# Kernel optimization log

Hardware: AMD Instinct MI355X
Metric: run time of the kernel (lower is better)

The kernel has to match this reference:

```python
import jax, jax.numpy as jnp
import numpy as np

VOCAB = 32000; DIM = 512; NL = 6; B = 2; L = 1024
DI = 2 * DIM      # d_inner (expand=2)
DS = 16           # d_state
DC = 4            # d_conv
DR = DIM // 16    # dt_rank = ceil(512/16) = 32


def setup_inputs() -> dict:
    key = jax.random.key(0)
    ks = jax.random.split(key, 10)
    s = 0.02
    tokens = jax.random.randint(ks[0], (B, L), 0, VOCAB)
    pos_emb = jax.random.normal(ks[1], (1, L, DIM)) * s
    embed = jax.random.normal(ks[2], (VOCAB, DIM)) * s
    lm_w = jax.random.normal(ks[3], (VOCAB, DIM)) * s
    lm_b = jnp.zeros((VOCAB,), jnp.float32)
    in_proj_w = jax.random.normal(ks[4], (NL, 2 * DI, DIM)) * s
    conv_w = jax.random.normal(ks[5], (NL, DI, DC)) * s
    conv_b = jnp.zeros((NL, DI), jnp.float32)
    x_proj_w = jax.random.normal(ks[6], (NL, DR + 2 * DS, DI)) * s
    dt_proj_w = jax.random.normal(ks[7], (NL, DI, DR)) * s
    dt_proj_b = jnp.broadcast_to(jnp.log(jnp.expm1(jnp.float32(0.01))), (NL, DI)).astype(jnp.float32)
    A_log = jnp.log(jnp.broadcast_to(jnp.arange(1, DS + 1, dtype=jnp.float32), (NL, DI, DS)))
    Dp = jnp.ones((NL, DI), jnp.float32)
    out_w = jax.random.normal(ks[8], (NL, DIM, DI)) * s
    ln_g = jnp.ones((NL, DIM), jnp.float32)
    ln_b = jnp.zeros((NL, DIM), jnp.float32)
    return dict(tokens=tokens, pos_emb=pos_emb, embed=embed, lm_w=lm_w, lm_b=lm_b,
                in_proj_w=in_proj_w, conv_w=conv_w, conv_b=conv_b, x_proj_w=x_proj_w,
                dt_proj_w=dt_proj_w, dt_proj_b=dt_proj_b, A_log=A_log, Dp=Dp,
                out_w=out_w, ln_g=ln_g, ln_b=ln_b)


def silu(x):
    return x * jax.nn.sigmoid(x)


def layernorm(x, g, b, eps=1e-5):
    mu = jnp.mean(x, -1, keepdims=True)
    var = jnp.var(x, -1, keepdims=True)
    return (x - mu) * jax.lax.rsqrt(var + eps) * g + b


def causal_dwconv(x, w, b):
    # x: (B,L,DI), w: (DI,DC) depthwise, left-pad causal
    xp = jnp.pad(x, ((0, 0), (DC - 1, 0), (0, 0)))
    y = b
    for k in range(DC):
        y = y + w[:, k] * xp[:, k:k + x.shape[1], :]
    return y


def selective_scan(u, dt, A, Bm, Cm, Dp):
    # u,dt: (B,L,DI); A: (DI,DS); Bm,Cm: (B,L,DS)
    dA = jnp.exp(dt[..., None] * A)                       # (B,L,DI,DS)
    dBu = dt[..., None] * Bm[:, :, None, :] * u[..., None]
    h0 = jnp.zeros((u.shape[0], DI, DS), u.dtype)

    def step(h, inp):
        dA_t, dBu_t, C_t = inp
        h = dA_t * h + dBu_t
        y = jnp.einsum('bdn,bn->bd', h, C_t)
        return h, y

    _, ys = jax.lax.scan(step, h0, (dA.transpose(1, 0, 2, 3),
                                    dBu.transpose(1, 0, 2, 3),
                                    Cm.transpose(1, 0, 2)))
    return ys.transpose(1, 0, 2) + u * Dp


def mamba_block(x, in_w, cw, cb, xp_w, dtw, dtb, A_log, Dp, ow):
    xz = jnp.einsum('bld,ed->ble', x, in_w)               # (B,L,2*DI)
    xc, z = jnp.split(xz, 2, axis=-1)
    xc = silu(causal_dwconv(xc, cw, cb))
    x_dbl = jnp.einsum('bld,ed->ble', xc, xp_w)           # (B,L,DR+2*DS)
    dt, Bm, Cm = jnp.split(x_dbl, [DR, DR + DS], axis=-1)
    dt = jax.nn.softplus(jnp.einsum('blr,dr->bld', dt, dtw) + dtb)
    A = -jnp.exp(A_log)
    y = selective_scan(xc, dt, A, Bm, Cm, Dp)
    y = y * silu(z)
    return jnp.einsum('bld,ed->ble', y, ow)


def reference(tokens, pos_emb, embed, lm_w, lm_b, in_proj_w, conv_w, conv_b,
              x_proj_w, dt_proj_w, dt_proj_b, A_log, Dp, out_w, ln_g, ln_b):
    x = embed[tokens] + pos_emb[:, :tokens.shape[1]]
    for i in range(NL):
        res = x
        x = mamba_block(x, in_proj_w[i], conv_w[i], conv_b[i], x_proj_w[i],
                        dt_proj_w[i], dt_proj_b[i], A_log[i], Dp[i], out_w[i])
        x = layernorm(x + res, ln_g[i], ln_b[i])
    return jnp.einsum('bld,vd->blv', x, lm_w) + lm_b
```

## Files before the change

### kernel.cpp

```cpp
#include <hip/hip_runtime.h>
#include <hip/hip_bf16.h>
#include <math.h>

#define BB 2
#define LL 1024
#define DIM 512
#define NL 6
#define DI 1024
#define DS 16
#define DC 4
#define DR 32
#define VOCAB 32000
#define M_ROWS (BB * LL)
#define CCH 64
#define CHLEN (LL / CCH)
#define KSPLIT 8
#define OSPLIT 4

typedef unsigned short u16;
typedef __attribute__((ext_vector_type(8))) short bf16x8;
typedef __attribute__((ext_vector_type(4))) float f32x4;

__device__ __forceinline__ u16 f2bf(float f) {
    unsigned u = __float_as_uint(f);
    u += 0x7FFF + ((u >> 16) & 1);
    return (u16)(u >> 16);
}
__device__ __forceinline__ float bf2f(u16 h) {
    return __uint_as_float(((unsigned)h) << 16);
}
#define SWZ(r, c) ((c) ^ (((r) >> 1) & 3))

__global__ __launch_bounds__(256) void cast_all(const float* __restrict__ lm,
                                                const float* __restrict__ inw,
                                                const float* __restrict__ ow,
                                                const float* __restrict__ xp,
                                                u16* __restrict__ lmb,
                                                u16* __restrict__ inb,
                                                u16* __restrict__ owb_,
                                                u16* __restrict__ xpb) {
    int idx = blockIdx.x * 256 + threadIdx.x;
    const float* src; u16* dst; int off;
    if (idx < 2048000)      { src = lm;  dst = lmb;  off = idx; }
    else if (idx < 2834432) { src = inw; dst = inb;  off = idx - 2048000; }
    else if (idx < 3227648) { src = ow;  dst = owb_; off = idx - 2834432; }
    else                    { src = xp;  dst = xpb;  off = idx - 3227648; }
    float4 v0 = ((const float4*)src)[off * 2];
    float4 v1 = ((const float4*)src)[off * 2 + 1];
    union { u16 h[8]; int4 v; } r;
    r.h[0] = f2bf(v0.x); r.h[1] = f2bf(v0.y); r.h[2] = f2bf(v0.z); r.h[3] = f2bf(v0.w);
    r.h[4] = f2bf(v1.x); r.h[5] = f2bf(v1.y); r.h[6] = f2bf(v1.z); r.h[7] = f2bf(v1.w);
    ((int4*)dst)[off] = r.v;
}

__global__ __launch_bounds__(256) void embed_kernel(const int* __restrict__ tok,
                                                    const float* __restrict__ pos,
                                                    const float* __restrict__ emb,
                                                    float* __restrict__ x,
                                                    u16* __restrict__ xb) {
    int idx = blockIdx.x * 256 + threadIdx.x;
    int d = idx & (DIM - 1);
    int l = (idx >> 9) & (LL - 1);
    int b = idx >> 19;
    int t = tok[b * LL + l];
    float v = emb[(size_t)t * DIM + d] + pos[l * DIM + d];
    x[idx] = v;
    xb[idx] = f2bf(v);
}

__global__ __launch_bounds__(256) void gemm_n64(const u16* __restrict__ A,
                                                const u16* __restrict__ W,
                                                float* __restrict__ out,
                                                u16* __restrict__ outb,
                                                const float* __restrict__ bias,
                                                int lda, int ldw, int ldc,
                                                int KS, int pstride) {
    __shared__ __align__(16) u16 As[2 * 4096];
    __shared__ __align__(16) u16 Ws[2 * 2048];
    const int t = threadIdx.x;
    const int l = t & 63;
    const int w = t >> 6;
    const int kz = blockIdx.x;
    const int bm = blockIdx.y * 128;
    const int bnn = blockIdx.z * 64;
    const int wm = w * 32;

    f32x4 acc[2][4] = {};
    const int nt = KS >> 5;
    const int kbeg = kz * KS;

    auto STAGE = [&](int bufi, int k0) {
#pragma unroll
        for (int p = 0; p < 2; ++p) {
            const int i = p * 256 + w * 64 + l;
            const int row = i >> 2;
            const int kq = SWZ(row, i & 3);
            __builtin_amdgcn_global_load_lds(
                (const __attribute__((address_space(1))) unsigned int*)
                    (A + (size_t)(bm + row) * lda + k0 + kq * 8),
                (__attribute__((address_space(3))) unsigned int*)
                    (As + bufi * 4096 + (p * 256 + w * 64) * 8),
                16, 0, 0);
        }
        {
            const int i = w * 64 + l;
            const int row = i >> 2;
            const int kq = SWZ(row, i & 3);
            __builtin_amdgcn_global_load_lds(
                (const __attribute__((address_space(1))) unsigned int*)
                    (W + (size_t)(bnn + row) * ldw + k0 + kq * 8),
                (__attribute__((address_space(3))) unsigned int*)
                    (Ws + bufi * 2048 + (w * 64) * 8),
                16, 0, 0);
        }
    };
    auto COMPUTE = [&](int bufi) {
        const u16* Ab = As + bufi * 4096;
        const u16* Wb = Ws + bufi * 2048;
#pragma unroll
        for (int mi = 0; mi < 2; ++mi) {
            const int ar = wm + mi * 16 + (l & 15);
            bf16x8 a = *(const bf16x8*)(Ab + ar * 32 + SWZ(ar, l >> 4) * 8);
#pragma unroll
            for (int ni = 0; ni < 4; ++ni) {
                const int wr = ni * 16 + (l & 15);
                bf16x8 b = *(const bf16x8*)(Wb + wr * 32 + SWZ(wr, l >> 4) * 8);
                acc[mi][ni] = __builtin_amdgcn_mfma_f32_16x16x32_bf16(b, a, acc[mi][ni], 0, 0, 0);
            }
        }
    };

    STAGE(0, kbeg);
    for (int tt = 0; tt < nt; ++tt) {
        if (tt + 1 < nt) {
            STAGE((tt + 1) & 1, kbeg + ((tt + 1) << 5));
            asm volatile("s_waitcnt vmcnt(3)\ns_barrier" ::: "memory");
        } else {
            asm volatile("s_waitcnt vmcnt(0)\ns_barrier" ::: "memory");
        }
        COMPUTE(tt & 1);
        asm volatile("s_waitcnt lgkmcnt(0)\ns_barrier" ::: "memory");
    }

    if (outb != nullptr) {
        u16* opb = outb + (size_t)kz * pstride;
#pragma unroll
        for (int mi = 0; mi < 2; ++mi) {
            const int row = bm + wm + mi * 16 + (l & 15);
#pragma unroll
            for (int ni = 0; ni < 4; ++ni) {
                const int col = bnn + ni * 16 + ((l >> 4) << 2);
                ushort4 v;
                v.x = f2bf(acc[mi][ni][0]); v.y = f2bf(acc[mi][ni][1]);
                v.z = f2bf(acc[mi][ni][2]); v.w = f2bf(acc[mi][ni][3]);
                *(ushort4*)(opb + (size_t)row * ldc + col) = v;
            }
        }
    } else {
        float* op = out + (size_t)kz * pstride;
#pragma unroll
        for (int mi = 0; mi < 2; ++mi) {
            const int row = bm + wm + mi * 16 + (l & 15);
#pragma unroll
            for (int ni = 0; ni < 4; ++ni) {
                const int col = bnn + ni * 16 + ((l >> 4) << 2);
                float4 v;
                v.x = acc[mi][ni][0]; v.y = acc[mi][ni][1];
                v.z = acc[mi][ni][2]; v.w = acc[mi][ni][3];
                if (bias != nullptr) {
                    float4 b4 = *(const float4*)(bias + col);
                    v.x += b4.x; v.y += b4.y; v.z += b4.z; v.w += b4.w;
                }
                *(float4*)(op + (size_t)row * ldc + col) = v;
            }
        }
    }
}

__global__ __launch_bounds__(256) void xdred_dt(const float* __restrict__ Pf,
                                                const float* __restrict__ dtw,
                                                const float* __restrict__ dtb,
                                                float* __restrict__ xd,
                                                float* __restrict__ dt) {
    __shared__ float xds[64];
    const int m = blockIdx.x;
    const int t = threadIdx.x;
    if (t < 64) {
        float s = 0.f;
#pragma unroll
        for (int kz = 0; kz < KSPLIT; ++kz)
            s += Pf[(size_t)kz * (M_ROWS * 64) + m * 64 + t];
        xds[t] = s;
        xd[m * 64 + t] = s;
    }
    __syncthreads();
    const int d0 = t * 4;
    const float4 bv = *(const float4*)(dtb + d0);
    float a0 = bv.x, a1 = bv.y, a2 = bv.z, a3 = bv.w;
    const float* w0p = dtw + (size_t)(d0 + 0) * DR;
    const float* w1p = dtw + (size_t)(d0 + 1) * DR;
    const float* w2p = dtw + (size_t)(d0 + 2) * DR;
    const float* w3p = dtw + (size_t)(d0 + 3) * DR;
#pragma unroll
    for (int k = 0; k < DR; k += 4) {
        float4 xv = *(const float4*)&xds[k];
        float4 w0 = *(const float4*)(w0p + k);
        float4 w1 = *(const float4*)(w1p + k);
        float4 w2 = *(const float4*)(w2p + k);
        float4 w3 = *(const float4*)(w3p + k);
        a0 += w0.x * xv.x + w0.y * xv.y + w0.z * xv.z + w0.w * xv.w;
        a1 += w1.x * xv.x + w1.y * xv.y + w1.z * xv.z + w1.w * xv.w;
        a2 += w2.x * xv.x + w2.y * xv.y + w2.z * xv.z + w2.w * xv.w;
        a3 += w3.x * xv.x + w3.y * xv.y + w3.z * xv.z + w3.w * xv.w;
    }
    a0 = (a0 > 20.f) ? a0 : log1pf(__expf(a0));
    a1 = (a1 > 20.f) ? a1 : log1pf(__expf(a1));
    a2 = (a2 > 20.f) ? a2 : log1pf(__expf(a2));
    a3 = (a3 > 20.f) ? a3 : log1pf(__expf(a3));
    float4 v; v.x = a0; v.y = a1; v.z = a2; v.w = a3;
    *(float4*)(dt + (size_t)m * DI + d0) = v;
}

__global__ __launch_bounds__(256) void conv_silu(const u16* __restrict__ xzb,
                                                 const float* __restrict__ cw,
                                                 const float* __restrict__ cb,
                                                 u16* __restrict__ xcb) {
    int idx = blockIdx.x * 256 + threadIdx.x;
    int c = idx & (DI - 1);
    int l = (idx >> 10) & (LL - 1);
    int b = idx >> 20;
    float acc = cb[c];
#pragma unroll
    for (int k = 0; k < DC; ++k) {
        int ll = l + k - (DC - 1);
        if (ll >= 0)
            acc += cw[c * DC + k] * bf2f(xzb[((size_t)(b * LL + ll)) * (2 * DI) + c]);
    }
    float v = acc / (1.f + __expf(-acc));
    xcb[idx] = f2bf(v);
}

__global__ __launch_bounds__(256) void scan_pass1(const u16* __restrict__ xcb,
                                                  const float* __restrict__ dt,
                                                  const float* __restrict__ xdbl,
                                                  const float* __restrict__ A_log,
                                                  float* __restrict__ S,
                                                  float* __restrict__ Q) {
    const int d = blockIdx.x * 256 + threadIdx.x;
    const int b = blockIdx.y;
    const int c = blockIdx.z;
    float a[DS];
#pragma unroll
    for (int q = 0; q < 4; ++q) {
        float4 al = *(const float4*)(A_log + d * DS + q * 4);
        a[q * 4 + 0] = -__expf(al.x);
        a[q * 4 + 1] = -__expf(al.y);
        a[q * 4 + 2] = -__expf(al.z);
        a[q * 4 + 3] = -__expf(al.w);
    }
    float Qr[DS];
#pragma unroll
    for (int n = 0; n < DS; ++n) Qr[n] = 0.f;
    float Ssum = 0.f;

    const int l0 = c * CHLEN;
    const float* dtp = dt + ((size_t)b * LL + l0) * DI + d;
    const u16*   up  = xcb + ((size_t)b * LL + l0) * DI + d;
    const float* xdp = xdbl + ((size_t)b * LL + l0) * 64 + DR;

    for (int l = 0; l < CHLEN; ++l) {
        float dtv = dtp[(size_t)l * DI];
        float uv  = bf2f(up[(size_t)l * DI]);
        float wv = dtv * uv;
        Ssum += dtv;
#pragma unroll
        for (int q = 0; q < 4; ++q) {
            float4 Bv = *(const float4*)(xdp + l * 64 + q * 4);
            float dA0 = __expf(dtv * a[q * 4 + 0]);
            float dA1 = __expf(dtv * a[q * 4 + 1]);
            float dA2 = __expf(dtv * a[q * 4 + 2]);
            float dA3 = __expf(dtv * a[q * 4 + 3]);
            Qr[q * 4 + 0] = dA0 * Qr[q * 4 + 0] + wv * Bv.x;
            Qr[q * 4 + 1] = dA1 * Qr[q * 4 + 1] + wv * Bv.y;
            Qr[q * 4 + 2] = dA2 * Qr[q * 4 + 2] + wv * Bv.z;
            Qr[q * 4 + 3] = dA3 * Qr[q * 4 + 3] + wv * Bv.w;
        }
    }
    S[((size_t)b * CCH + c) * DI + d] = Ssum;
    float* Qp = Q + (((size_t)b * CCH + c) * DI + d) * DS;
#pragma unroll
    for (int q = 0; q < 4; ++q) {
        float4 o;
        o.x = Qr[q * 4 + 0]; o.y = Qr[q * 4 + 1];
        o.z = Qr[q * 4 + 2]; o.w = Qr[q * 4 + 3];
        *(float4*)(Qp + q * 4) = o;
    }
}

__global__ __launch_bounds__(64) void scan_pass2(const float* __restrict__ A_log,
                                                 const float* __restrict__ S,
                                                 float* __restrict__ Q) {
    const int idx = blockIdx.x * 64 + threadIdx.x;
    const int b = idx >> 14;
    const int dn = idx & 16383;
    const int d = dn >> 4;
    const float a = -__expf(A_log[dn]);
    float h = 0.f;
    for (int c = 0; c < CCH; ++c) {
        const size_t soff = ((size_t)b * CCH + c) * DI + d;
        const size_t qoff = ((size_t)b * CCH + c) * (size_t)(DI * DS) + dn;
        float P = __expf(a * S[soff]);
        float qv = Q[qoff];
        Q[qoff] = h;
        h = P * h + qv;
    }
}

__global__ __launch_bounds__(256) void scan_pass3(const u16* __restrict__ xcb,
                                                  const float* __restrict__ dt,
                                                  const float* __restrict__ xdbl,
                                                  const u16* __restrict__ xzb,
                                                  const float* __restrict__ A_log,
                                                  const float* __restrict__ Dpp,
                                                  const float* __restrict__ Q,
                                                  u16* __restrict__ y) {
    const int d = blockIdx.x * 256 + threadIdx.x;
    const int b = blockIdx.y;
    const int c = blockIdx.z;
    float a[DS];
#pragma unroll
    for (int q = 0; q < 4; ++q) {
        float4 al = *(const float4*)(A_log + d * DS + q * 4);
        a[q * 4 + 0] = -__expf(al.x);
        a[q * 4 + 1] = -__expf(al.y);
        a[q * 4 + 2] = -__expf(al.z);
        a[q * 4 + 3] = -__expf(al.w);
    }
    float h[DS];
    const float* Qp = Q + (((size_t)b * CCH + c) * DI + d) * DS;
#pragma unroll
    for (int q = 0; q < 4; ++q) {
        float4 hv = *(const float4*)(Qp + q * 4);
        h[q * 4 + 0] = hv.x; h[q * 4 + 1] = hv.y;
        h[q * 4 + 2] = hv.z; h[q * 4 + 3] = hv.w;
    }
    const float dp = Dpp[d];

    const int l0 = c * CHLEN;
    const float* dtp = dt + ((size_t)b * LL + l0) * DI + d;
    const u16*   up  = xcb + ((size_t)b * LL + l0) * DI + d;
    const float* xdp = xdbl + ((size_t)b * LL + l0) * 64 + DR;
    const u16* zp = xzb + ((size_t)b * LL + l0) * (2 * DI) + DI + d;
    u16* yp = y + ((size_t)b * LL + l0) * DI + d;

    for (int l = 0; l < CHLEN; ++l) {
        float dtv = dtp[(size_t)l * DI];
        float uv  = bf2f(up[(size_t)l * DI]);
        float wv = dtv * uv;
        float p = 0.f;
#pragma unroll
        for (int q = 0; q < 4; ++q) {
            float4 Bv = *(const float4*)(xdp + l * 64 + q * 4);
            float4 Cv = *(const float4*)(xdp + l * 64 + 16 + q * 4);
            float dA0 = __expf(dtv * a[q * 4 + 0]);
            float dA1 = __expf(dtv * a[q * 4 + 1]);
            float dA2 = __expf(dtv * a[q * 4 + 2]);
            float dA3 = __expf(dtv * a[q * 4 + 3]);
            h[q * 4 + 0] = dA0 * h[q * 4 + 0] + wv * Bv.x;
            h[q * 4 + 1] = dA1 * h[q * 4 + 1] + wv * Bv.y;
            h[q * 4 + 2] = dA2 * h[q * 4 + 2] + wv * Bv.z;
            h[q * 4 + 3] = dA3 * h[q * 4 + 3] + wv * Bv.w;
            p += h[q * 4 + 0] * Cv.x + h[q * 4 + 1] * Cv.y +
                 h[q * 4 + 2] * Cv.z + h[q * 4 + 3] * Cv.w;
        }
        float zv = bf2f(zp[(size_t)l * (2 * DI)]);
        float g = zv / (1.f + __expf(-zv));
        yp[(size_t)l * DI] = f2bf((p + uv * dp) * g);
    }
}

__global__ __launch_bounds__(256) void add_ln(const float* __restrict__ opart,
                                              float* __restrict__ x,
                                              const float* __restrict__ g,
                                              const float* __restrict__ b,
                                              u16* __restrict__ xb) {
    const int PS = M_ROWS * DIM;
    int m = blockIdx.x;
    int t = threadIdx.x;
    const float* xr = x + (size_t)m * DIM;
    float v0 = xr[t];
    float v1 = xr[t + 256];
#pragma unroll
    for (int kz = 0; kz < OSPLIT; ++kz) {
        const float* op = opart + (size_t)kz * PS + (size_t)m * DIM;
        v0 += op[t];
        v1 += op[t + 256];
    }
    float s = v0 + v1;
    float ss = v0 * v0 + v1 * v1;
#pragma unroll
    for (int off = 32; off > 0; off >>= 1) {
        s += __shfl_down(s, off, 64);
        ss += __shfl_down(ss, off, 64);
    }
    __shared__ float sb[4], ssb[4];
    int w = t >> 6;
    if ((t & 63) == 0) { sb[w] = s; ssb[w] = ss; }
    __syncthreads();
    float stot = sb[0] + sb[1] + sb[2] + sb[3];
    float sstot = ssb[0] + ssb[1] + ssb[2] + ssb[3];
    float mean = stot * (1.f / DIM);
    float var = sstot * (1.f / DIM) - mean * mean;
    float rs = rsqrtf(var + 1e-5f);
    float* xw = x + (size_t)m * DIM;
    float o0 = (v0 - mean) * rs * g[t] + b[t];
    float o1 = (v1 - mean) * rs * g[t + 256] + b[t + 256];
    xw[t] = o0;
    xw[t + 256] = o1;
    xb[(size_t)m * DIM + t] = f2bf(o0);
    xb[(size_t)m * DIM + t + 256] = f2bf(o1);
}

extern "C" void kernel_launch(void* const* d_in, const int* in_sizes, int n_in,
                              void* d_out, int out_size, void* d_ws, size_t ws_size,
                              hipStream_t stream) {
    const int*   tokens = (const int*)d_in[0];
    const float* pos    = (const float*)d_in[1];
    const float* emb    = (const float*)d_in[2];
    const float* lm_w   = (const float*)d_in[3];
    const float* lm_b   = (const float*)d_in[4];
    const float* in_w   = (const float*)d_in[5];
    const float* cw     = (const float*)d_in[6];
    const float* cb     = (const float*)d_in[7];
    const float* xpw    = (const float*)d_in[8];
    const float* dtw    = (const float*)d_in[9];
    const float* dtb    = (const float*)d_in[10];
    const float* A_log  = (const float*)d_in[11];
    const float* Dpp    = (const float*)d_in[12];
    const float* ow     = (const float*)d_in[13];
    const float* lng    = (const float*)d_in[14];
    const float* lnb    = (const float*)d_in[15];
    float* out = (float*)d_out;

    float* ws = (float*)d_ws;
    float* x    = ws;
    float* xd   = x + 1048576;
    float* dt   = xd + 131072;
    float* S    = dt + 2097152;
    float* Qb   = S + 131072;
    float* Pf   = Qb + 2097152;
    float* Pf2  = Pf + 1048576;
    u16* xzb    = (u16*)(Pf2 + 4194304);
    u16* xb     = xzb + 4194304;
    u16* yb     = xb + 1048576;
    u16* xcb    = yb + 2097152;
    u16* lm_wb  = xcb + 2097152;
    u16* in_wb  = lm_wb + 16384000;
    u16* owb    = in_wb + 6291456;
    u16* xpwb   = owb + 3145728;

    cast_all<<<12800, 256, 0, stream>>>(lm_w, in_w, ow, xpw,
                                        lm_wb, in_wb, owb, xpwb);

    embed_kernel<<<M_ROWS * DIM / 256, 256, 0, stream>>>(tokens, pos, emb, x, xb);

    for (int i = 0; i < NL; ++i) {
        gemm_n64<<<dim3(1, M_ROWS / 128, 2048 / 64), 256, 0, stream>>>(
            xb, in_wb + (size_t)i * 2048 * 512, nullptr, xzb, nullptr,
            512, 512, 2048, 512, 0);
        conv_silu<<<M_ROWS * DI / 256, 256, 0, stream>>>(
            xzb, cw + (size_t)i * DI * DC, cb + (size_t)i * DI, xcb);
        gemm_n64<<<dim3(KSPLIT, M_ROWS / 128, 1), 256, 0, stream>>>(
            xcb, xpwb + (size_t)i * 64 * 1024, Pf, nullptr, nullptr,
            1024, 1024, 64, 1024 / KSPLIT, M_ROWS * 64);
        xdred_dt<<<M_ROWS, 256, 0, stream>>>(
            Pf, dtw + (size_t)i * DI * DR, dtb + (size_t)i * DI, xd, dt);
        scan_pass1<<<dim3(DI / 256, BB, CCH), 256, 0, stream>>>(
            xcb, dt, xd, A_log + (size_t)i * DI * DS, S, Qb);
        scan_pass2<<<(BB * DI * DS) / 64, 64, 0, stream>>>(
            A_log + (size_t)i * DI * DS, S, Qb);
        scan_pass3<<<dim3(DI / 256, BB, CCH), 256, 0, stream>>>(
            xcb, dt, xd, xzb, A_log + (size_t)i * DI * DS, Dpp + (size_t)i * DI, Qb, yb);
        gemm_n64<<<dim3(OSPLIT, M_ROWS / 128, 512 / 64), 256, 0, stream>>>(
            yb, owb + (size_t)i * 512 * 1024, Pf2, nullptr, nullptr,
            1024, 1024, 512, 1024 / OSPLIT, M_ROWS * 512);
        add_ln<<<M_ROWS, 256, 0, stream>>>(
            Pf2, x, lng + (size_t)i * DIM, lnb + (size_t)i * DIM, xb);
    }

    gemm_n64<<<dim3(1, M_ROWS / 128, VOCAB / 64), 256, 0, stream>>>(
        xb, lm_wb, out, nullptr, lm_b,
        512, 512, VOCAB, 512, 0);
}
```

Measured before the change: 841.8 us.

## Remap GEMM workgroups across XCDs and stage fp32 epilogue through LDS

Workgroup IDs are remapped so that consecutive logical tiles land on the same XCD, which is meant to improve L2 reuse of shared A and W tiles. The fp32 output epilogue now writes accumulators into an LDS tile (padded stride of 65 floats), then reads them back row-contiguously for coalesced float4 global stores with bias added. This mainly targets the large LM-head output write. In exchange it adds barriers and reuses the operand LDS buffers. The 65-float stride also leaves the float4 LDS accesses not 16-byte aligned, which may split those accesses or cause a correctness risk.

```diff
diff --git a/kernel.cpp b/kernel.cpp
--- a/kernel.cpp
+++ b/kernel.cpp
@@ -75,14 +75,23 @@
                                                 const float* __restrict__ bias,
                                                 int lda, int ldw, int ldc,
                                                 int KS, int pstride) {
-    __shared__ __align__(16) u16 As[2 * 4096];
-    __shared__ __align__(16) u16 Ws[2 * 2048];
+    __shared__ __align__(16) char smem_raw[24576];
+    u16* As = (u16*)smem_raw;
+    u16* Ws = (u16*)(smem_raw + 16384);
+    float* Cs = (float*)smem_raw;
+
     const int t = threadIdx.x;
     const int l = t & 63;
     const int w = t >> 6;
-    const int kz = blockIdx.x;
-    const int bm = blockIdx.y * 128;
-    const int bnn = blockIdx.z * 64;
+    const int gx = gridDim.x, gy = gridDim.y;
+    const int nwg = gx * gy * gridDim.z;
+    const int fid = (blockIdx.z * gy + blockIdx.y) * gx + blockIdx.x;
+    const int q8 = nwg >> 3, r8 = nwg & 7;
+    const int xcd = fid & 7, rank = fid >> 3;
+    const int wgid = (xcd < r8 ? xcd * (q8 + 1) : r8 * (q8 + 1) + (xcd - r8) * q8) + rank;
+    const int kz = wgid % gx;
+    const int bm = ((wgid / gx) % gy) * 128;
+    const int bnn = (wgid / (gx * gy)) * 64;
     const int wm = w * 32;
 
     f32x4 acc[2][4] = {};
@@ -159,20 +168,36 @@
     } else {
         float* op = out + (size_t)kz * pstride;
 #pragma unroll
-        for (int mi = 0; mi < 2; ++mi) {
-            const int row = bm + wm + mi * 16 + (l & 15);
-#pragma unroll
-            for (int ni = 0; ni < 4; ++ni) {
-                const int col = bnn + ni * 16 + ((l >> 4) << 2);
-                float4 v;
-                v.x = acc[mi][ni][0]; v.y = acc[mi][ni][1];
-                v.z = acc[mi][ni][2]; v.w = acc[mi][ni][3];
+        for (int pass = 0; pass < 2; ++pass) {
+            if ((w >> 1) == pass) {
+                const int rbase = (w & 1) * 32;
+#pragma unroll
+                for (int mi = 0; mi < 2; ++mi) {
+                    const int r = rbase + mi * 16 + (l & 15);
+#pragma unroll
+                    for (int ni = 0; ni < 4; ++ni) {
+                        const int c = ni * 16 + ((l >> 4) << 2);
+                        float4 v;
+                        v.x = acc[mi][ni][0]; v.y = acc[mi][ni][1];
+                        v.z = acc[mi][ni][2]; v.w = acc[mi][ni][3];
+                        *(float4*)(Cs + r * 65 + c) = v;
+                    }
+                }
+            }
+            __syncthreads();
+#pragma unroll
+            for (int it = 0; it < 4; ++it) {
+                const int idx = it * 256 + t;
+                const int r = idx >> 4;
+                const int c4 = (idx & 15) * 4;
+                float4 v = *(float4*)(Cs + r * 65 + c4);
                 if (bias != nullptr) {
-                    float4 b4 = *(const float4*)(bias + col);
+                    float4 b4 = *(const float4*)(bias + bnn + c4);
                     v.x += b4.x; v.y += b4.y; v.z += b4.z; v.w += b4.w;
                 }
-                *(float4*)(op + (size_t)row * ldc + col) = v;
+                *(float4*)(op + (size_t)(bm + pass * 64 + r) * ldc + bnn + c4) = v;
             }
+            __syncthreads();
         }
     }
 }
```

After: 851.1 us. No clear change (+1.1%).
